# Kernel tuning notes

Hardware: AMD Instinct MI355X
Metric: run time of the kernel (lower is better)

Reference implementation:

```python
import jax, jax.numpy as jnp
import numpy as np

B, T, C, HEADS = 4, 2305, 384, 6
BN_EPS = 1e-5


def setup_inputs() -> dict:
    key = jax.random.key(0)
    ks = jax.random.split(key, 24)
    d = {
        'x': jax.random.normal(ks[0], (B, T, C), dtype=jnp.float32),
        'h': 48,
        'w': 48,
        # depthwise conv kernels (groups=C, no bias): OIHW with I=1
        'kq': jax.random.normal(ks[1], (C, 1, 3, 3), dtype=jnp.float32) * 0.1,
        'kk': jax.random.normal(ks[2], (C, 1, 3, 3), dtype=jnp.float32) * 0.1,
        'kv': jax.random.normal(ks[3], (C, 1, 3, 3), dtype=jnp.float32) * 0.1,
        # BatchNorm (eval mode) params per projection: gamma, beta, running_mean, running_var
        'gq': jax.random.normal(ks[4], (C,), dtype=jnp.float32) * 0.1 + 1.0,
        'bq': jax.random.normal(ks[5], (C,), dtype=jnp.float32) * 0.1,
        'mq': jax.random.normal(ks[6], (C,), dtype=jnp.float32) * 0.1,
        'vq': jax.random.uniform(ks[7], (C,), dtype=jnp.float32) + 0.5,
        'gk': jax.random.normal(ks[8], (C,), dtype=jnp.float32) * 0.1 + 1.0,
        'bk': jax.random.normal(ks[9], (C,), dtype=jnp.float32) * 0.1,
        'mk': jax.random.normal(ks[10], (C,), dtype=jnp.float32) * 0.1,
        'vk': jax.random.uniform(ks[11], (C,), dtype=jnp.float32) + 0.5,
        'gv': jax.random.normal(ks[12], (C,), dtype=jnp.float32) * 0.1 + 1.0,
        'bv': jax.random.normal(ks[13], (C,), dtype=jnp.float32) * 0.1,
        'mv': jax.random.normal(ks[14], (C,), dtype=jnp.float32) * 0.1,
        'vv': jax.random.uniform(ks[15], (C,), dtype=jnp.float32) + 0.5,
        # Linear weights, torch convention [out, in]; qkv_bias=False
        'Wq': jax.random.normal(ks[16], (C, C), dtype=jnp.float32) / np.sqrt(C),
        'Wk': jax.random.normal(ks[17], (C, C), dtype=jnp.float32) / np.sqrt(C),
        'Wv': jax.random.normal(ks[18], (C, C), dtype=jnp.float32) / np.sqrt(C),
        'Wo': jax.random.normal(ks[19], (C, C), dtype=jnp.float32) / np.sqrt(C),
        'bo': jax.random.normal(ks[20], (C,), dtype=jnp.float32) * 0.01,
    }
    return d


def _dw_bn(xi, kern, gamma, beta, mean, var, h, w):
    # xi: [B, C, h, w]; depthwise 3x3 conv, stride 1, pad 1, then eval-mode BN
    y = jax.lax.conv_general_dilated(
        xi, kern, window_strides=(1, 1), padding=((1, 1), (1, 1)),
        feature_group_count=C, dimension_numbers=('NCHW', 'OIHW', 'NCHW'))
    scale = (gamma / jnp.sqrt(var + BN_EPS))[None, :, None, None]
    y = (y - mean[None, :, None, None]) * scale + beta[None, :, None, None]
    # b c h w -> b (h w) c
    return y.transpose(0, 2, 3, 1).reshape(y.shape[0], h * w, C)


def _forward(x, kq, kk, kv, gq, bq, mq, vq, gk, bk, mk, vk, gv, bv, mv, vv,
             Wq, Wk, Wv, Wo, bo, h, w):
    b, t, c = x.shape
    scale = c ** (-0.5)  # note: dim**-0.5, NOT head_dim**-0.5 (as in source)
    cls_tok, xs = x[:, :1], x[:, 1:]
    xi = xs.reshape(b, h, w, c).transpose(0, 3, 1, 2)  # b (h w) c -> b c h w
    q = jnp.concatenate([cls_tok, _dw_bn(xi, kq, gq, bq, mq, vq, h, w)], axis=1)
    k = jnp.concatenate([cls_tok, _dw_bn(xi, kk, gk, bk, mk, vk, h, w)], axis=1)
    v = jnp.concatenate([cls_tok, _dw_bn(xi, kv, gv, bv, mv, vv, h, w)], axis=1)
    dh = c // HEADS
    q = (q @ Wq.T).reshape(b, t, HEADS, dh).transpose(0, 2, 1, 3)  # bhtd
    k = (k @ Wk.T).reshape(b, t, HEADS, dh).transpose(0, 2, 1, 3)
    v = (v @ Wv.T).reshape(b, t, HEADS, dh).transpose(0, 2, 1, 3)
    attn = jax.nn.softmax(jnp.einsum('bhld,bhtd->bhlt', q, k) * scale, axis=-1)
    out = jnp.einsum('bhlt,bhtd->bhld', attn, v)
    out = out.transpose(0, 2, 1, 3).reshape(b, t, c)
    return out @ Wo.T + bo


def reference(x, kq, kk, kv, gq, bq, mq, vq, gk, bk, mk, vk, gv, bv, mv, vv,
              Wq, Wk, Wv, Wo, bo, h, w):
    return _forward(x, kq, kk, kv, gq, bq, mq, vq, gk, bk, mk, vk, gv, bv,
                    mv, vv, Wq, Wk, Wv, Wo, bo, h, w)
```

## Files before the change

### kernel.cpp

```cpp
#include <hip/hip_runtime.h>
#include <hip/hip_bf16.h>

#define BN 4
#define TT 2305
#define CC 384
#define HH 6
#define DH 64
#define GW 48
#define BH (BN*HH)
#define TP 2368
#define TQP 2560
#define MF 9220
#define MP 9344
#define MB2 73
#define NSPL 2
#define C2 0.07362223f

typedef __hip_bfloat16 bf16;
typedef __attribute__((ext_vector_type(8))) short short8;
typedef __attribute__((ext_vector_type(4))) float floatx4;
typedef __attribute__((ext_vector_type(16))) float floatx16;

#define MFMA16(a,b,c) __builtin_amdgcn_mfma_f32_16x16x32_bf16((a),(b),(c),0,0,0)
#define MFMA32(a,b,c) __builtin_amdgcn_mfma_f32_32x32x16_bf16((a),(b),(c),0,0,0)

__device__ __forceinline__ unsigned pack2(float a, float b) {
    bf16 lo = __float2bfloat16(a);
    bf16 hi = __float2bfloat16(b);
    unsigned short ul = *reinterpret_cast<unsigned short*>(&lo);
    unsigned short uh = *reinterpret_cast<unsigned short*>(&hi);
    return (unsigned)ul | ((unsigned)uh << 16);
}
__device__ __forceinline__ float bu2f(unsigned u16) {
    unsigned v = u16 << 16;
    return *reinterpret_cast<float*>(&v);
}

__global__ __launch_bounds__(384)
void conv_bn(const float* __restrict__ x,
             const float* __restrict__ kq, const float* __restrict__ kk, const float* __restrict__ kv,
             const float* __restrict__ gq, const float* __restrict__ bq, const float* __restrict__ mq, const float* __restrict__ vq,
             const float* __restrict__ gk, const float* __restrict__ bk, const float* __restrict__ mk, const float* __restrict__ vk,
             const float* __restrict__ gv, const float* __restrict__ bv, const float* __restrict__ mv, const float* __restrict__ vv,
             const float* __restrict__ Wq, const float* __restrict__ Wk,
             const float* __restrict__ Wv, const float* __restrict__ Wo,
             bf16* __restrict__ wqb, bf16* __restrict__ wkb,
             bf16* __restrict__ wvb, bf16* __restrict__ wob,
             bf16* __restrict__ cq, bf16* __restrict__ ck, bf16* __restrict__ cv)
{
    {
        const int i = blockIdx.x * 384 + threadIdx.x;
        if (i < CC * CC) {
            wqb[i] = __float2bfloat16(Wq[i]);
            wkb[i] = __float2bfloat16(Wk[i]);
            wvb[i] = __float2bfloat16(Wv[i]);
            wob[i] = __float2bfloat16(Wo[i]);
        }
    }

    const int n = blockIdx.x;
    const int b = n / 289;
    const int t0 = (n % 289) * 8;
    const int c = threadIdx.x;
    const size_t xbase = (size_t)b * TT * CC;

    const float sq = gq[c] * rsqrtf(vq[c] + 1e-5f), oq = bq[c] - mq[c] * sq;
    const float sk = gk[c] * rsqrtf(vk[c] + 1e-5f), ok = bk[c] - mk[c] * sk;
    const float sv = gv[c] * rsqrtf(vv[c] + 1e-5f), ov = bv[c] - mv[c] * sv;
    float wq9[9], wk9[9], wv9[9];
    #pragma unroll
    for (int u = 0; u < 9; u++) {
        wq9[u] = kq[c * 9 + u]; wk9[u] = kk[c * 9 + u]; wv9[u] = kv[c * 9 + u];
    }

    for (int g = 0; g < 8; g++) {
        const int t = t0 + g;
        if (t >= TT) break;
        const size_t mrow = (size_t)(b * TT + t) * CC + c;
        if (t == 0) {
            bf16 xv = __float2bfloat16(x[xbase + c]);
            cq[mrow] = xv; ck[mrow] = xv; cv[mrow] = xv;
        } else {
            const int s = t - 1, i = s / GW, j = s % GW;
            float aq = 0.f, ak = 0.f, av = 0.f;
            #pragma unroll
            for (int di = 0; di < 3; di++) {
                int ii = i + di - 1;
                if (ii < 0 || ii >= GW) continue;
                #pragma unroll
                for (int dj = 0; dj < 3; dj++) {
                    int jj = j + dj - 1;
                    if (jj < 0 || jj >= GW) continue;
                    float xv = x[xbase + (size_t)(1 + ii * GW + jj) * CC + c];
                    int u = di * 3 + dj;
                    aq += xv * wq9[u]; ak += xv * wk9[u]; av += xv * wv9[u];
                }
            }
            cq[mrow] = __float2bfloat16(aq * sq + oq);
            ck[mrow] = __float2bfloat16(ak * sk + ok);
            cv[mrow] = __float2bfloat16(av * sv + ov);
        }
    }
}

__global__ __launch_bounds__(256)
void qkv_gemm(const bf16* __restrict__ cq, const bf16* __restrict__ ck, const bf16* __restrict__ cv,
              const bf16* __restrict__ Wq, const bf16* __restrict__ Wk, const bf16* __restrict__ Wv,
              bf16* __restrict__ q, bf16* __restrict__ k, bf16* __restrict__ vT)
{
    const int bt = blockIdx.x;
    const int b = bt / 10;
    const int m0 = (bt % 10) * 256;
    const int n0 = blockIdx.y * 64;
    const int w = threadIdx.x >> 6, lane = threadIdx.x & 63;
    const int lm = lane & 15, q4 = lane >> 4;
    const int which = n0 / CC;
    const int obase = n0 % CC;
    const bf16* A = (which == 0) ? cq : (which == 1) ? ck : cv;
    const bf16* W = (which == 0) ? Wq : (which == 1) ? Wk : Wv;

    __shared__ __align__(16) bf16 TR[64 * 264];

    size_t arow[4];
    #pragma unroll
    for (int st = 0; st < 4; st++) {
        int t = m0 + st * 64 + w * 16 + lm;
        if (t >= TT) t = TT - 1;
        arow[st] = (size_t)(b * TT + t) * CC;
    }

    floatx4 acc[4][4];
    #pragma unroll
    for (int st = 0; st < 4; st++)
        #pragma unroll
        for (int n = 0; n < 4; n++) acc[st][n] = (floatx4){0.f, 0.f, 0.f, 0.f};

    #pragma unroll 2
    for (int kc = 0; kc < CC / 32; kc++) {
        short8 a[4];
        #pragma unroll
        for (int st = 0; st < 4; st++)
            a[st] = *(const short8*)(A + arow[st] + kc * 32 + q4 * 8);
        #pragma unroll
        for (int n = 0; n < 4; n++) {
            short8 bfr = *(const short8*)(W + (size_t)(obase + n * 16 + lm) * CC + kc * 32 + q4 * 8);
            #pragma unroll
            for (int st = 0; st < 4; st++)
                acc[st][n] = MFMA16(a[st], bfr, acc[st][n]);
        }
    }

    if (which == 2) {
        #pragma unroll
        for (int st = 0; st < 4; st++)
            #pragma unroll
            for (int n = 0; n < 4; n++) {
                const int ol = n * 16 + lm;
                const int ml = st * 64 + w * 16 + q4 * 4;
                uint2 pkd = { pack2(acc[st][n][0], acc[st][n][1]),
                              pack2(acc[st][n][2], acc[st][n][3]) };
                *(uint2*)&TR[ol * 264 + ml] = pkd;
            }
        __syncthreads();
        const int h = obase >> 6;
        const int o = threadIdx.x >> 2;
        const int seg = threadIdx.x & 3;
        const size_t vrow = ((size_t)(b * HH + h) * DH + o) * TP;
        #pragma unroll
        for (int j = 0; j < 8; j++) {
            const int ml = seg * 64 + j * 8;
            const int t = m0 + ml;
            uint4 val = *(const uint4*)&TR[o * 264 + ml];
            if (t + 8 <= TT) {
                *(uint4*)(vT + vrow + t) = val;
            } else if (t < TT) {
                const bf16* pv = (const bf16*)&val;
                for (int e = 0; e < 8 && t + e < TT; e++) vT[vrow + t + e] = pv[e];
            }
        }
    } else {
        #pragma unroll
        for (int st = 0; st < 4; st++)
            #pragma unroll
            for (int n = 0; n < 4; n++) {
                const int o = obase + n * 16 + lm;
                const int h = o >> 6, d = o & 63;
                #pragma unroll
                for (int r = 0; r < 4; r++) {
                    const int t = m0 + st * 64 + w * 16 + q4 * 4 + r;
                    if (t >= TT) continue;
                    bf16 val = __float2bfloat16(acc[st][n][r]);
                    if (which == 0)
                        q[((size_t)(b * HH + h) * TQP + t) * DH + d] = val;
                    else
                        k[((size_t)(b * HH + h) * TP + t) * DH + d] = val;
                }
            }
    }
}

__global__ __launch_bounds__(256, 2)
void flash(const bf16* __restrict__ q, const bf16* __restrict__ k,
           const bf16* __restrict__ vT, bf16* __restrict__ OP, float* __restrict__ ML)
{
    const int id = blockIdx.x;
    const int bh = id % BH;
    const int rest = id / BH;
    const int z = rest % NSPL;
    const int qt = rest / NSPL;
    const int tid = threadIdx.x;
    const int w = tid >> 6, lane = tid & 63;
    const int q31 = lane & 31, hh = lane >> 5;
    const int q0 = qt * 256 + w * 64;
    const size_t kbase = (size_t)bh * TP * DH;
    const size_t qbase = (size_t)bh * TQP * DH;

    short8 qf[2][4];
    #pragma unroll
    for (int s = 0; s < 2; s++) {
        const bf16* qrow = q + qbase + (size_t)(q0 + s * 32 + q31) * DH;
        #pragma unroll
        for (int kc = 0; kc < 4; kc++)
            qf[s][kc] = *(const short8*)(qrow + kc * 16 + hh * 8);
    }

    floatx16 of[2][2];
    #pragma unroll
    for (int s = 0; s < 2; s++)
        #pragma unroll
        for (int dt = 0; dt < 2; dt++)
            #pragma unroll
            for (int r = 0; r < 16; r++) of[s][dt][r] = 0.f;
    float m2[2] = {-1e30f, -1e30f}, lsum[2] = {0.f, 0.f};

    const int tstart = z ? 19 : 0;
    const int tend   = z ? 37 : 19;

    for (int tc = tstart; tc < tend; tc++) {
        const int t0 = tc * 64;
        const bf16* kt = k + kbase + (size_t)t0 * DH;
        const bf16* vt = vT + kbase + t0;

        short8 ka[2][4], va[2][4];
        #pragma unroll
        for (int mt = 0; mt < 2; mt++)
            #pragma unroll
            for (int kc = 0; kc < 4; kc++) {
                const int row = mt * 32 + q31, c = 2 * kc + hh;
                ka[mt][kc] = *(const short8*)(kt + (size_t)row * DH + c * 8);
                va[mt][kc] = *(const short8*)(vt + (size_t)row * TP + c * 8);
            }
        const bool tail = (t0 + 64 > TT);

        #pragma unroll
        for (int s = 0; s < 2; s++) {
            floatx16 sv[2];
            #pragma unroll
            for (int mt = 0; mt < 2; mt++)
                #pragma unroll
                for (int r = 0; r < 16; r++) sv[mt][r] = 0.f;
            #pragma unroll
            for (int kc = 0; kc < 4; kc++) {
                sv[0] = MFMA32(ka[0][kc], qf[s][kc], sv[0]);
                sv[1] = MFMA32(ka[1][kc], qf[s][kc], sv[1]);
            }
            if (tail) {
                #pragma unroll
                for (int mt = 0; mt < 2; mt++)
                    #pragma unroll
                    for (int r = 0; r < 16; r++) {
                        const int tl = t0 + mt * 32 + (r & 3) + 8 * (r >> 2) + 4 * hh;
                        if (tl >= TT) sv[mt][r] = -1e30f;
                    }
            }
            float rm = sv[0][0];
            #pragma unroll
            for (int r = 1; r < 16; r++) rm = fmaxf(rm, sv[0][r]);
            #pragma unroll
            for (int r = 0; r < 16; r++) rm = fmaxf(rm, sv[1][r]);
            rm = fmaxf(rm, __shfl_xor(rm, 32));
            const float mn = fmaxf(m2[s], rm * C2);
            const float alpha = __builtin_amdgcn_exp2f(m2[s] - mn);
            m2[s] = mn;
            const float negm = -mn;
            float rs = 0.f;
            unsigned pk[2][8];
            #pragma unroll
            for (int mt = 0; mt < 2; mt++)
                #pragma unroll
                for (int p = 0; p < 8; p++) {
                    const float p0 = __builtin_amdgcn_exp2f(fmaf(sv[mt][2 * p], C2, negm));
                    const float p1 = __builtin_amdgcn_exp2f(fmaf(sv[mt][2 * p + 1], C2, negm));
                    rs += p0 + p1;
                    pk[mt][p] = pack2(p0, p1);
                }
            rs += __shfl_xor(rs, 32);
            lsum[s] = lsum[s] * alpha + rs;
            #pragma unroll
            for (int dt = 0; dt < 2; dt++)
                #pragma unroll
                for (int r = 0; r < 16; r++) of[s][dt][r] *= alpha;

            #pragma unroll
            for (int kc = 0; kc < 4; kc++) {
                const int u0 = 2 * kc, u1 = 2 * kc + 1;
                const unsigned P0a = pk[u0 >> 2][2 * (u0 & 3)];
                const unsigned P0b = pk[u0 >> 2][2 * (u0 & 3) + 1];
                const unsigned P1a = pk[u1 >> 2][2 * (u1 & 3)];
                const unsigned P1b = pk[u1 >> 2][2 * (u1 & 3) + 1];
                const unsigned X1 = hh ? P0a : P1a;
                const unsigned X2 = hh ? P0b : P1b;
                const unsigned Y1 = __shfl_xor(X1, 32);
                const unsigned Y2 = __shfl_xor(X2, 32);
                unsigned dw[4];
                dw[0] = hh ? Y1 : P0a;
                dw[1] = hh ? Y2 : P0b;
                dw[2] = hh ? P1a : Y1;
                dw[3] = hh ? P1b : Y2;
                short8 pb = *reinterpret_cast<short8*>(dw);
                of[s][0] = MFMA32(va[0][kc], pb, of[s][0]);
                of[s][1] = MFMA32(va[1][kc], pb, of[s][1]);
            }
        }
    }

    #pragma unroll
    for (int s = 0; s < 2; s++) {
        const int qrow = q0 + s * 32 + q31;
        if (qrow >= TT) continue;
        bf16* orow = OP + ((size_t)(z * BH + bh) * TT + qrow) * DH;
        #pragma unroll
        for (int dt = 0; dt < 2; dt++)
            #pragma unroll
            for (int p = 0; p < 4; p++) {
                const int d = dt * 32 + 8 * p + 4 * hh;
                unsigned lo = pack2(of[s][dt][4 * p], of[s][dt][4 * p + 1]);
                unsigned hi = pack2(of[s][dt][4 * p + 2], of[s][dt][4 * p + 3]);
                uint2 st = {lo, hi};
                *(uint2*)(orow + d) = st;
            }
        if (hh == 0) {
            float2 ml = {m2[s], lsum[s]};
            *(float2*)&ML[((size_t)(z * BH + bh) * TT + qrow) * 2] = ml;
        }
    }
}

__global__ __launch_bounds__(256)
void merge(const bf16* __restrict__ OP, const float* __restrict__ ML,
           bf16* __restrict__ att)
{
    const int idx = blockIdx.x * 256 + threadIdx.x;
    if (idx >= BH * TT * 16) return;
    const int quad = idx & 15;
    const int pair = idx >> 4;
    const int bh = pair / TT, row = pair % TT;
    const int b = bh / HH, h = bh % HH;
    const int d0 = quad * 4;

    float2 ml[NSPL];
    #pragma unroll
    for (int z = 0; z < NSPL; z++)
        ml[z] = *(const float2*)&ML[((size_t)(z * BH + bh) * TT + row) * 2];
    float M = ml[0].x;
    #pragma unroll
    for (int z = 1; z < NSPL; z++) M = fmaxf(M, ml[z].x);
    float wz[NSPL], den = 0.f;
    #pragma unroll
    for (int z = 0; z < NSPL; z++) {
        wz[z] = __builtin_amdgcn_exp2f(ml[z].x - M);
        den += ml[z].y * wz[z];
    }
    const float inv = 1.f / den;

    float o0 = 0.f, o1 = 0.f, o2 = 0.f, o3 = 0.f;
    #pragma unroll
    for (int z = 0; z < NSPL; z++) {
        const float s = wz[z] * inv;
        const uint2 a = *(const uint2*)&OP[((size_t)(z * BH + bh) * TT + row) * DH + d0];
        o0 += bu2f(a.x & 0xffffu) * s;
        o1 += bu2f(a.x >> 16)     * s;
        o2 += bu2f(a.y & 0xffffu) * s;
        o3 += bu2f(a.y >> 16)     * s;
    }
    uint2 st = {pack2(o0, o1), pack2(o2, o3)};
    *(uint2*)&att[((size_t)(b * TT + row) * CC) + h * DH + d0] = st;
}

__global__ __launch_bounds__(256)
void out_gemm(const bf16* __restrict__ att, const bf16* __restrict__ Wo_bf,
              const float* __restrict__ bo, float* __restrict__ out)
{
    const int m0 = blockIdx.x * 128;
    const int n0 = blockIdx.y * 64;
    const int w = threadIdx.x >> 6, lane = threadIdx.x & 63;
    const int lm = lane & 15, q4 = lane >> 4;

    const size_t ar0 = (size_t)(m0 + w * 16 + lm) * CC;
    floatx4 acc[2][4];
    #pragma unroll
    for (int st = 0; st < 2; st++)
        #pragma unroll
        for (int n = 0; n < 4; n++) acc[st][n] = (floatx4){0.f, 0.f, 0.f, 0.f};

    #pragma unroll 4
    for (int kc = 0; kc < CC / 32; kc++) {
        short8 a0 = *(const short8*)(att + ar0 + kc * 32 + q4 * 8);
        short8 a1 = *(const short8*)(att + ar0 + (size_t)64 * CC + kc * 32 + q4 * 8);
        #pragma unroll
        for (int n = 0; n < 4; n++) {
            short8 bfr = *(const short8*)(Wo_bf + (size_t)(n0 + n * 16 + lm) * CC + kc * 32 + q4 * 8);
            acc[0][n] = MFMA16(a0, bfr, acc[0][n]);
            acc[1][n] = MFMA16(a1, bfr, acc[1][n]);
        }
    }

    #pragma unroll
    for (int st = 0; st < 2; st++)
        #pragma unroll
        for (int n = 0; n < 4; n++) {
            const int o = n0 + n * 16 + lm;
            const float bias = bo[o];
            #pragma unroll
            for (int r = 0; r < 4; r++) {
                const int m = m0 + st * 64 + w * 16 + q4 * 4 + r;
                if (m < MF) out[(size_t)m * CC + o] = acc[st][n][r] + bias;
            }
        }
}

extern "C" void kernel_launch(void* const* d_in, const int* in_sizes, int n_in,
                              void* d_out, int out_size, void* d_ws, size_t ws_size,
                              hipStream_t stream)
{
    const float* x  = (const float*)d_in[0];
    const float* kq = (const float*)d_in[3];
    const float* kk = (const float*)d_in[4];
    const float* kv = (const float*)d_in[5];
    const float* gq = (const float*)d_in[6];
    const float* bq = (const float*)d_in[7];
    const float* mq = (const float*)d_in[8];
    const float* vq = (const float*)d_in[9];
    const float* gk = (const float*)d_in[10];
    const float* bk = (const float*)d_in[11];
    const float* mk = (const float*)d_in[12];
    const float* vk = (const float*)d_in[13];
    const float* gv = (const float*)d_in[14];
    const float* bv = (const float*)d_in[15];
    const float* mv = (const float*)d_in[16];
    const float* vv = (const float*)d_in[17];
    const float* Wq = (const float*)d_in[18];
    const float* Wk = (const float*)d_in[19];
    const float* Wv = (const float*)d_in[20];
    const float* Wo = (const float*)d_in[21];
    const float* bo = (const float*)d_in[22];

    char* ws = (char*)d_ws;
    const size_t SZ_CONV = (size_t)MP * CC * 2;
    const size_t SZ_Q    = (size_t)BH * TQP * DH * 2;
    const size_t SZ_K    = (size_t)BH * TP * DH * 2;
    const size_t SZ_W    = (size_t)CC * CC * 2;
    size_t off = 0;
    bf16* cq   = (bf16*)(ws + off); off += SZ_CONV;
    bf16* ck   = (bf16*)(ws + off); off += SZ_CONV;
    bf16* cv   = (bf16*)(ws + off); off += SZ_CONV;
    bf16* qb   = (bf16*)(ws + off); off += SZ_Q;
    bf16* kb   = (bf16*)(ws + off); off += SZ_K;
    bf16* vTb  = (bf16*)(ws + off); off += SZ_K;
    bf16* attb = (bf16*)(ws + off); off += SZ_CONV;
    bf16* wqb  = (bf16*)(ws + off); off += SZ_W;
    bf16* wkb  = (bf16*)(ws + off); off += SZ_W;
    bf16* wvb  = (bf16*)(ws + off); off += SZ_W;
    bf16* wob  = (bf16*)(ws + off); off += SZ_W;
    bf16*  OP = (bf16*)ws;
    float* ML = (float*)(ws + off); off += (size_t)NSPL * BH * TT * 2 * 4;

    conv_bn<<<BN * 289, 384, 0, stream>>>(x, kq, kk, kv,
                                          gq, bq, mq, vq,
                                          gk, bk, mk, vk,
                                          gv, bv, mv, vv,
                                          Wq, Wk, Wv, Wo,
                                          wqb, wkb, wvb, wob,
                                          cq, ck, cv);
    qkv_gemm<<<dim3(40, 18), 256, 0, stream>>>(cq, ck, cv, wqb, wkb, wvb, qb, kb, vTb);
    flash<<<10 * NSPL * BH, 256, 0, stream>>>(qb, kb, vTb, OP, ML);
    merge<<<(BH * TT * 16 + 255) / 256, 256, 0, stream>>>(OP, ML, attb);
    out_gemm<<<dim3(MB2, 6), 256, 0, stream>>>(attb, wob, bo, (float*)d_out);
}
```

Measured before the change: 283.1 us.

## Shrink flash attention tile to 32 query rows per wave for higher occupancy

Each wave in the flash kernel now handles 32 query rows instead of 64. Blocks cover 128 queries, so the grid grows from 10 to 19 query tiles. Dropping the second query sub-tile halves the accumulator and fragment registers, and launch bounds are raised to 4 blocks per CU. K and V fragments are now loaded just before use rather than preloaded. In exchange, each K/V load is reused by half as many queries, which doubles K/V global traffic, and load latency is exposed closer to the MFMAs.

After: 351.0 us. 1.24x slower.

```diff
diff --git a/kernel.cpp b/kernel.cpp
--- a/kernel.cpp
+++ b/kernel.cpp
@@ -14,6 +14,7 @@
 #define MP 9344
 #define MB2 73
 #define NSPL 2
+#define NQT 19
 #define C2 0.07362223f
 
 typedef __hip_bfloat16 bf16;
@@ -199,7 +200,7 @@
     }
 }
 
-__global__ __launch_bounds__(256, 2)
+__global__ __launch_bounds__(256, 4)
 void flash(const bf16* __restrict__ q, const bf16* __restrict__ k,
            const bf16* __restrict__ vT, bf16* __restrict__ OP, float* __restrict__ ML)
 {
@@ -211,27 +212,24 @@
     const int tid = threadIdx.x;
     const int w = tid >> 6, lane = tid & 63;
     const int q31 = lane & 31, hh = lane >> 5;
-    const int q0 = qt * 256 + w * 64;
+    const int q0 = qt * 128 + w * 32;
     const size_t kbase = (size_t)bh * TP * DH;
     const size_t qbase = (size_t)bh * TQP * DH;
 
-    short8 qf[2][4];
-    #pragma unroll
-    for (int s = 0; s < 2; s++) {
-        const bf16* qrow = q + qbase + (size_t)(q0 + s * 32 + q31) * DH;
+    short8 qf[4];
+    {
+        const bf16* qrow = q + qbase + (size_t)(q0 + q31) * DH;
         #pragma unroll
         for (int kc = 0; kc < 4; kc++)
-            qf[s][kc] = *(const short8*)(qrow + kc * 16 + hh * 8);
-    }
-
-    floatx16 of[2][2];
-    #pragma unroll
-    for (int s = 0; s < 2; s++)
-        #pragma unroll
-        for (int dt = 0; dt < 2; dt++)
-            #pragma unroll
-            for (int r = 0; r < 16; r++) of[s][dt][r] = 0.f;
-    float m2[2] = {-1e30f, -1e30f}, lsum[2] = {0.f, 0.f};
+            qf[kc] = *(const short8*)(qrow + kc * 16 + hh * 8);
+    }
+
+    floatx16 of[2];
+    #pragma unroll
+    for (int dt = 0; dt < 2; dt++)
+        #pragma unroll
+        for (int r = 0; r < 16; r++) of[dt][r] = 0.f;
+    float m2 = -1e30f, lsum = 0.f;
 
     const int tstart = z ? 19 : 0;
     const int tend   = z ? 37 : 19;
@@ -241,106 +239,99 @@
         const bf16* kt = k + kbase + (size_t)t0 * DH;
         const bf16* vt = vT + kbase + t0;
 
-        short8 ka[2][4], va[2][4];
-        #pragma unroll
-        for (int mt = 0; mt < 2; mt++)
-            #pragma unroll
-            for (int kc = 0; kc < 4; kc++) {
-                const int row = mt * 32 + q31, c = 2 * kc + hh;
-                ka[mt][kc] = *(const short8*)(kt + (size_t)row * DH + c * 8);
-                va[mt][kc] = *(const short8*)(vt + (size_t)row * TP + c * 8);
-            }
-        const bool tail = (t0 + 64 > TT);
-
-        #pragma unroll
-        for (int s = 0; s < 2; s++) {
-            floatx16 sv[2];
+        floatx16 sv[2];
+        #pragma unroll
+        for (int mt = 0; mt < 2; mt++) {
+            #pragma unroll
+            for (int r = 0; r < 16; r++) sv[mt][r] = 0.f;
+            const int row = mt * 32 + q31;
+            short8 ka0 = *(const short8*)(kt + (size_t)row * DH + (2 * 0 + hh) * 8);
+            short8 ka1 = *(const short8*)(kt + (size_t)row * DH + (2 * 1 + hh) * 8);
+            short8 ka2 = *(const short8*)(kt + (size_t)row * DH + (2 * 2 + hh) * 8);
+            short8 ka3 = *(const short8*)(kt + (size_t)row * DH + (2 * 3 + hh) * 8);
+            sv[mt] = MFMA32(ka0, qf[0], sv[mt]);
+            sv[mt] = MFMA32(ka1, qf[1], sv[mt]);
+            sv[mt] = MFMA32(ka2, qf[2], sv[mt]);
+            sv[mt] = MFMA32(ka3, qf[3], sv[mt]);
+        }
+        if (t0 + 64 > TT) {
             #pragma unroll
             for (int mt = 0; mt < 2; mt++)
                 #pragma unroll
-                for (int r = 0; r < 16; r++) sv[mt][r] = 0.f;
-            #pragma unroll
-            for (int kc = 0; kc < 4; kc++) {
-                sv[0] = MFMA32(ka[0][kc], qf[s][kc], sv[0]);
-                sv[1] = MFMA32(ka[1][kc], qf[s][kc], sv[1]);
-            }
-            if (tail) {
-                #pragma unroll
-                for (int mt = 0; mt < 2; mt++)
-                    #pragma unroll
-                    for (int r = 0; r < 16; r++) {
-                        const int tl = t0 + mt * 32 + (r & 3) + 8 * (r >> 2) + 4 * hh;
-                        if (tl >= TT) sv[mt][r] = -1e30f;
-                    }
-            }
-            float rm = sv[0][0];
-            #pragma unroll
-            for (int r = 1; r < 16; r++) rm = fmaxf(rm, sv[0][r]);
-            #pragma unroll
-            for (int r = 0; r < 16; r++) rm = fmaxf(rm, sv[1][r]);
-            rm = fmaxf(rm, __shfl_xor(rm, 32));
-            const float mn = fmaxf(m2[s], rm * C2);
-            const float alpha = __builtin_amdgcn_exp2f(m2[s] - mn);
-            m2[s] = mn;
-            const float negm = -mn;
-            float rs = 0.f;
-            unsigned pk[2][8];
-            #pragma unroll
-            for (int mt = 0; mt < 2; mt++)
-                #pragma unroll
-                for (int p = 0; p < 8; p++) {
-                    const float p0 = __builtin_amdgcn_exp2f(fmaf(sv[mt][2 * p], C2, negm));
-                    const float p1 = __builtin_amdgcn_exp2f(fmaf(sv[mt][2 * p + 1], C2, negm));
-                    rs += p0 + p1;
-                    pk[mt][p] = pack2(p0, p1);
+                for (int r = 0; r < 16; r++) {
+                    const int tl = t0 + mt * 32 + (r & 3) + 8 * (r >> 2) + 4 * hh;
+                    if (tl >= TT) sv[mt][r] = -1e30f;
                 }
-            rs += __shfl_xor(rs, 32);
-            lsum[s] = lsum[s] * alpha + rs;
-            #pragma unroll
-            for (int dt = 0; dt < 2; dt++)
-                #pragma unroll
-                for (int r = 0; r < 16; r++) of[s][dt][r] *= alpha;
-
-            #pragma unroll
-            for (int kc = 0; kc < 4; kc++) {
-                const int u0 = 2 * kc, u1 = 2 * kc + 1;
-                const unsigned P0a = pk[u0 >> 2][2 * (u0 & 3)];
-                const unsigned P0b = pk[u0 >> 2][2 * (u0 & 3) + 1];
-                const unsigned P1a = pk[u1 >> 2][2 * (u1 & 3)];
-                const unsigned P1b = pk[u1 >> 2][2 * (u1 & 3) + 1];
-                const unsigned X1 = hh ? P0a : P1a;
-                const unsigned X2 = hh ? P0b : P1b;
-                const unsigned Y1 = __shfl_xor(X1, 32);
-                const unsigned Y2 = __shfl_xor(X2, 32);
-                unsigned dw[4];
-                dw[0] = hh ? Y1 : P0a;
-                dw[1] = hh ? Y2 : P0b;
-                dw[2] = hh ? P1a : Y1;
-                dw[3] = hh ? P1b : Y2;
-                short8 pb = *reinterpret_cast<short8*>(dw);
-                of[s][0] = MFMA32(va[0][kc], pb, of[s][0]);
-                of[s][1] = MFMA32(va[1][kc], pb, of[s][1]);
-            }
-        }
-    }
-
-    #pragma unroll
-    for (int s = 0; s < 2; s++) {
-        const int qrow = q0 + s * 32 + q31;
-        if (qrow >= TT) continue;
+        }
+
+        float rm = sv[0][0];
+        #pragma unroll
+        for (int r = 1; r < 16; r++) rm = fmaxf(rm, sv[0][r]);
+        #pragma unroll
+        for (int r = 0; r < 16; r++) rm = fmaxf(rm, sv[1][r]);
+        rm = fmaxf(rm, __shfl_xor(rm, 32));
+        const float mn = fmaxf(m2, rm * C2);
+        const float alpha = __builtin_amdgcn_exp2f(m2 - mn);
+        m2 = mn;
+        const float negm = -mn;
+        float rs = 0.f;
+        unsigned pk[2][8];
+        #pragma unroll
+        for (int mt = 0; mt < 2; mt++)
+            #pragma unroll
+            for (int p = 0; p < 8; p++) {
+                const float p0 = __builtin_amdgcn_exp2f(fmaf(sv[mt][2 * p], C2, negm));
+                const float p1 = __builtin_amdgcn_exp2f(fmaf(sv[mt][2 * p + 1], C2, negm));
+                rs += p0 + p1;
+                pk[mt][p] = pack2(p0, p1);
+            }
+        rs += __shfl_xor(rs, 32);
+        lsum = lsum * alpha + rs;
+        #pragma unroll
+        for (int dt = 0; dt < 2; dt++)
+            #pragma unroll
+            for (int r = 0; r < 16; r++) of[dt][r] *= alpha;
+
+        #pragma unroll
+        for (int kc = 0; kc < 4; kc++) {
+            const int u0 = 2 * kc, u1 = 2 * kc + 1;
+            const unsigned P0a = pk[u0 >> 2][2 * (u0 & 3)];
+            const unsigned P0b = pk[u0 >> 2][2 * (u0 & 3) + 1];
+            const unsigned P1a = pk[u1 >> 2][2 * (u1 & 3)];
+            const unsigned P1b = pk[u1 >> 2][2 * (u1 & 3) + 1];
+            const unsigned X1 = hh ? P0a : P1a;
+            const unsigned X2 = hh ? P0b : P1b;
+            const unsigned Y1 = __shfl_xor(X1, 32);
+            const unsigned Y2 = __shfl_xor(X2, 32);
+            unsigned dw[4];
+            dw[0] = hh ? Y1 : P0a;
+            dw[1] = hh ? Y2 : P0b;
+            dw[2] = hh ? P1a : Y1;
+            dw[3] = hh ? P1b : Y2;
+            short8 pb = *reinterpret_cast<short8*>(dw);
+            const int c = 2 * kc + hh;
+            short8 va0 = *(const short8*)(vt + (size_t)(q31) * TP + c * 8);
+            short8 va1 = *(const short8*)(vt + (size_t)(32 + q31) * TP + c * 8);
+            of[0] = MFMA32(va0, pb, of[0]);
+            of[1] = MFMA32(va1, pb, of[1]);
+        }
+    }
+
+    const int qrow = q0 + q31;
+    if (qrow < TT) {
         bf16* orow = OP + ((size_t)(z * BH + bh) * TT + qrow) * DH;
         #pragma unroll
         for (int dt = 0; dt < 2; dt++)
             #pragma unroll
             for (int p = 0; p < 4; p++) {
                 const int d = dt * 32 + 8 * p + 4 * hh;
-                unsigned lo = pack2(of[s][dt][4 * p], of[s][dt][4 * p + 1]);
-                unsigned hi = pack2(of[s][dt][4 * p + 2], of[s][dt][4 * p + 3]);
+                unsigned lo = pack2(of[dt][4 * p], of[dt][4 * p + 1]);
+                unsigned hi = pack2(of[dt][4 * p + 2], of[dt][4 * p + 3]);
                 uint2 st = {lo, hi};
                 *(uint2*)(orow + d) = st;
             }
         if (hh == 0) {
-            float2 ml = {m2[s], lsum[s]};
+            float2 ml = {m2, lsum};
             *(float2*)&ML[((size_t)(z * BH + bh) * TT + qrow) * 2] = ml;
         }
     }
@@ -483,7 +474,7 @@
                                           wqb, wkb, wvb, wob,
                                           cq, ck, cv);
     qkv_gemm<<<dim3(40, 18), 256, 0, stream>>>(cq, ck, cv, wqb, wkb, wvb, qb, kb, vTb);
-    flash<<<10 * NSPL * BH, 256, 0, stream>>>(qb, kb, vTb, OP, ML);
+    flash<<<NQT * NSPL * BH, 256, 0, stream>>>(qb, kb, vTb, OP, ML);
     merge<<<(BH * TT * 16 + 255) / 256, 256, 0, stream>>>(OP, ML, attb);
     out_gemm<<<dim3(MB2, 6), 256, 0, stream>>>(attb, wob, bo, (float*)d_out);
 }
```
